# Optimization experiments

Hardware: AMD Instinct MI355X
Metric: run time of the kernel (lower is better)

The kernel has to match this reference:

```python
import jax, jax.numpy as jnp
import numpy as np

BS = 2048   # batch, iterated sequentially (memory carried step to step)
M = 256     # memory_size
E = 128     # expanded_memory_emb_size
HS = 512    # summarizer_hidden_size
HA = 512    # shared_AC_hidden_size
HP = 256    # processor_hidden_size


def make_pe(max_len, d):
    # standard sinusoidal positional encoding [max_len, d]
    pos = np.arange(max_len, dtype=np.float32)[:, None]
    div = np.exp(np.arange(0, d, 2, dtype=np.float32) * (-np.log(10000.0) / d))
    pe = np.zeros((max_len, d), dtype=np.float32)
    pe[:, 0::2] = np.sin(pos * div)
    pe[:, 1::2] = np.cos(pos * div)
    return jnp.asarray(pe)


def setup_inputs() -> dict:
    key = jax.random.key(0)
    ks = jax.random.split(key, 32)

    def n(k, sh, s=0.05):
        return jax.random.normal(k, sh, dtype=jnp.float32) * s

    return {
        "state": jax.random.normal(ks[0], (BS, 4), dtype=jnp.float32),
        "memory0": jax.random.uniform(ks[1], (M, E), dtype=jnp.float32),  # buffer init U(0,1)
        # embedder: Linear(4, E)
        "W_emb": n(ks[2], (4, E)), "b_emb": n(ks[3], (E,)),
        # reader Summarizer MLP: E -> HS -> 1
        "Wr1": n(ks[4], (E, HS)), "br1": n(ks[5], (HS,)),
        "Wr2": n(ks[6], (HS, 1)), "br2": n(ks[7], (1,)),
        # writer Summarizer MLP: E -> HS -> M
        "Ww1": n(ks[8], (E, HS)), "bw1": n(ks[9], (HS,)),
        "Ww2": n(ks[10], (HS, M)), "bw2": n(ks[11], (M,)),
        # shared AC trunk: 2E -> HA
        "Ws": n(ks[12], (2 * E, HA)), "bs_": n(ks[13], (HA,)),
        # actor: HA -> 5, critic: HA -> 1
        "Wa": n(ks[14], (HA, 5)), "ba": n(ks[15], (5,)),
        "Wc": n(ks[16], (HA, 1)), "bc": n(ks[17], (1,)),
        # processor: (5 + 1 + 2E) -> HP -> E
        "Wp1": n(ks[18], (5 + 1 + 2 * E, HP)), "bp1": n(ks[19], (HP,)),
        "Wp2": n(ks[20], (HP, E)), "bp2": n(ks[21], (E,)),
    }


def reference(state, memory0, W_emb, b_emb, Wr1, br1, Wr2, br2,
              Ww1, bw1, Ww2, bw2, Ws, bs_, Wa, ba, Wc, bc,
              Wp1, bp1, Wp2, bp2):
    pe_mem = make_pe(M, E)  # PE added to the M memory slots
    sg = jax.lax.stop_gradient

    def summarize(x, W1, b1, W2, b2):
        # Summarizer (MLP method): weight = softmax over token axis, z = weight^T x
        w = jax.nn.softmax(jax.nn.relu(x @ W1 + b1) @ W2 + b2, axis=0)  # [T, K]
        return w.T @ x  # [K, E]

    se = state @ W_emb + b_emb  # embed once: [BS, E]

    def step(mem, s):
        # reader over [current state ; PE(memory)] -> single summary token
        xr = jnp.concatenate([s[None, :], mem + pe_mem], axis=0)        # [M+1, E]
        mem_state = summarize(xr, Wr1, br1, Wr2, br2)[0]                # [E]
        cstate = jnp.concatenate([s, mem_state])                        # concat=True -> [2E]
        h = jax.nn.relu(cstate @ Ws + bs_)                              # [HA]
        probs = jax.nn.softmax(h @ Wa + ba)                             # [5]
        val = h @ Wc + bc                                               # [1]
        pin = jnp.concatenate([s, mem_state, probs, val])               # [2E+6]
        ms2 = jax.nn.relu(pin @ Wp1 + bp1) @ Wp2 + bp2                  # processed mem_state [E]
        # writer sees detached state / mem_state / memory (torch .detach())
        xw = jnp.concatenate([sg(s)[None, :], sg(ms2)[None, :], sg(mem) + pe_mem], axis=0)  # [M+2, E]
        nm = summarize(xw, Ww1, bw1, Ww2, bw2)                          # [M, E]
        nm = nm - nm.min(axis=-1, keepdims=True)
        nm = nm / nm.max(axis=-1, keepdims=True)
        return nm, (probs, val)

    _, (action_probs, state_values) = jax.lax.scan(step, memory0, se)
    return action_probs, state_values  # [BS, 5], [BS, 1]
```

## Files before the change

kernel.cpp:

```cpp
#include <hip/hip_runtime.h>
#include <math.h>

#define BSZ 2048
#define MM  256
#define EE  128
#define HSS 512
#define HPP 256
#define NOWN 64
#define NBLK 129
#define LEADER 128
#define TPB 512
#define ROWS 4

typedef float f4 __attribute__((ext_vector_type(4)));

#define OFF_PE   512
#define OFF_R0   (OFF_PE + MM*EE)
#define OFF_W0   (OFF_R0 + BSZ)
#define OFF_MP   (OFF_W0 + BSZ*MM)
#define OFF_SW   (OFF_MP + 2*MM*EE)
#define OFF_EV   (OFF_SW + 2*MM*MM)
#define OFF_ES   (OFF_EV + NOWN*EE)
#define OFF_MS2  (OFF_ES + NOWN)
#define OFF_CS   (OFF_MS2 + EE)
#define OFF_CBS  (OFF_CS + 4*HSS)
#define OFF_CP   (OFF_CBS + HSS)
#define OFF_CBP  (OFF_CP + 4*HPP)
#define OFF_BD   (OFF_CBP + HPP)
#define OFF_BP   (OFF_BD + NOWN*ROWS)

struct KParams {
  const float *state, *mem0, *Wemb, *bemb, *Wr1, *br1, *Wr2, *br2;
  const float *Ww1, *bw1, *Ww2, *bw2, *Ws, *bs, *Wa, *ba, *Wc, *bc;
  const float *Wp1, *bp1, *Wp2, *bp2;
  float *out;
  float *ws;
};

__device__ __forceinline__ float ldA(const float* p) {
  return __hip_atomic_load(p, __ATOMIC_RELAXED, __HIP_MEMORY_SCOPE_AGENT);
}
__device__ __forceinline__ void stA(float* p, float v) {
  __hip_atomic_store(p, v, __ATOMIC_RELAXED, __HIP_MEMORY_SCOPE_AGENT);
}
__device__ __forceinline__ unsigned ldAu(const unsigned* p) {
  return __hip_atomic_load(p, __ATOMIC_RELAXED, __HIP_MEMORY_SCOPE_AGENT);
}
__device__ __forceinline__ void stAu(unsigned* p, unsigned v) {
  __hip_atomic_store(p, v, __ATOMIC_RELAXED, __HIP_MEMORY_SCOPE_AGENT);
}

__device__ __forceinline__ void ldA4x8(const float* p, int strideF, f4* v) {
  const float *p1=p+strideF, *p2=p+2*strideF, *p3=p+3*strideF,
              *p4=p+4*strideF, *p5=p+5*strideF, *p6=p+6*strideF, *p7=p+7*strideF;
  asm volatile(
    "global_load_dwordx4 %0, %8, off sc0 sc1\n\t"
    "global_load_dwordx4 %1, %9, off sc0 sc1\n\t"
    "global_load_dwordx4 %2, %10, off sc0 sc1\n\t"
    "global_load_dwordx4 %3, %11, off sc0 sc1\n\t"
    "global_load_dwordx4 %4, %12, off sc0 sc1\n\t"
    "global_load_dwordx4 %5, %13, off sc0 sc1\n\t"
    "global_load_dwordx4 %6, %14, off sc0 sc1\n\t"
    "global_load_dwordx4 %7, %15, off sc0 sc1\n\t"
    "s_waitcnt vmcnt(0)"
    : "=&v"(v[0]), "=&v"(v[1]), "=&v"(v[2]), "=&v"(v[3]),
      "=&v"(v[4]), "=&v"(v[5]), "=&v"(v[6]), "=&v"(v[7])
    : "v"(p), "v"(p1), "v"(p2), "v"(p3), "v"(p4), "v"(p5), "v"(p6), "v"(p7)
    : "memory");
}
__device__ __forceinline__ void ldA4x4(const float* p, int strideF, f4* v) {
  const float *p1=p+strideF, *p2=p+2*strideF, *p3=p+3*strideF;
  asm volatile(
    "global_load_dwordx4 %0, %4, off sc0 sc1\n\t"
    "global_load_dwordx4 %1, %5, off sc0 sc1\n\t"
    "global_load_dwordx4 %2, %6, off sc0 sc1\n\t"
    "global_load_dwordx4 %3, %7, off sc0 sc1\n\t"
    "s_waitcnt vmcnt(0)"
    : "=&v"(v[0]), "=&v"(v[1]), "=&v"(v[2]), "=&v"(v[3])
    : "v"(p), "v"(p1), "v"(p2), "v"(p3)
    : "memory");
}
__device__ __forceinline__ f4 ldA4(const float* p) {
  f4 r;
  asm volatile("global_load_dwordx4 %0, %1, off sc0 sc1\n\ts_waitcnt vmcnt(0)"
    : "=&v"(r) : "v"(p) : "memory");
  return r;
}

__device__ __forceinline__ void drainSync() {
  asm volatile("s_waitcnt vmcnt(0)" ::: "memory");
  __syncthreads();
}

__device__ __forceinline__ float brs(float v, float* s8, int tid) {
  for (int o = 32; o > 0; o >>= 1) v += __shfl_down(v, o, 64);
  __syncthreads();
  if ((tid & 63) == 0) s8[tid >> 6] = v;
  __syncthreads();
  float r = s8[0]+s8[1]+s8[2]+s8[3]+s8[4]+s8[5]+s8[6]+s8[7];
  __syncthreads();
  return r;
}

template<int N>
__device__ __forceinline__ void brsN(float* v, float* sred, int tid) {
  #pragma unroll
  for (int k = 0; k < N; ++k)
    for (int o = 32; o > 0; o >>= 1) v[k] += __shfl_down(v[k], o, 64);
  __syncthreads();
  if ((tid & 63) == 0) {
    const int w = tid >> 6;
    #pragma unroll
    for (int k = 0; k < N; ++k) sred[k*8 + w] = v[k];
  }
  __syncthreads();
  #pragma unroll
  for (int k = 0; k < N; ++k) {
    float s = sred[k*8 + 0];
    #pragma unroll
    for (int w = 1; w < 8; ++w) s += sred[k*8 + w];
    v[k] = s;
  }
  __syncthreads();
}

__global__ __launch_bounds__(TPB)
void toyac_kernel(KParams p) {
  const int g = blockIdx.x;
  const int tid = threadIdx.x;
  float* ws = p.ws;
  unsigned* bar = (unsigned*)p.ws;
  const int og = (g >= NOWN && g < LEADER) ? (g - NOWN) : g;
  const int c0 = ROWS * ((g < NOWN) ? g : og);

  __shared__ float sX[ROWS][EE];
  __shared__ float sBuf[8192];
  __shared__ float sH4[ROWS][HSS];
  __shared__ float sHms[HSS];
  __shared__ float sEv[ROWS][MM];
  __shared__ float sRed[16];
  __shared__ float s8[8];
  __shared__ float sR48[48];
  __shared__ float sMS[EE];
  __shared__ float sMS2[EE];
  __shared__ float sSE[EE];
  __shared__ float sP1[HPP];
  __shared__ float sHv[HSS];
  __shared__ float sD[ROWS];
  __shared__ float sSm[32];

  const int hq = (tid & 127) * 4;
  const int eg4 = tid >> 7;

  if (g < NOWN) {
    const int e = tid & 127, r = tid >> 7, c = c0 + r;
    double dv = exp(-(double)(2*(e>>1)) * log(10000.0) / 128.0);
    double arg = (double)c * dv;
    float pev = ((e & 1) == 0) ? (float)sin(arg) : (float)cos(arg);
    ws[OFF_PE + (size_t)c*EE + e] = pev;
    float m0v = p.mem0[(size_t)c*EE + e] + pev;
    stA(ws + OFF_MP + (size_t)c*EE + e, m0v);
    sX[r][e] = m0v;
  } else if (g == LEADER) {
    for (int jj = tid; jj < HSS; jj += TPB) {
      float a0=0.f,a1=0.f,a2=0.f,a3=0.f,cb=0.f;
      for (int e = 0; e < EE; ++e) {
        float wv = p.Ws[(size_t)e*HSS + jj];
        a0 += p.Wemb[e]*wv; a1 += p.Wemb[EE+e]*wv;
        a2 += p.Wemb[2*EE+e]*wv; a3 += p.Wemb[3*EE+e]*wv;
        cb += p.bemb[e]*wv;
      }
      ws[OFF_CS + jj] = a0; ws[OFF_CS + HSS + jj] = a1;
      ws[OFF_CS + 2*HSS + jj] = a2; ws[OFF_CS + 3*HSS + jj] = a3;
      ws[OFF_CBS + jj] = cb;
    }
    if (tid < HPP) {
      int k = tid;
      float a0=0.f,a1=0.f,a2=0.f,a3=0.f,cb=0.f;
      for (int e = 0; e < EE; ++e) {
        float wv = p.Wp1[(size_t)e*HPP + k];
        a0 += p.Wemb[e]*wv; a1 += p.Wemb[EE+e]*wv;
        a2 += p.Wemb[2*EE+e]*wv; a3 += p.Wemb[3*EE+e]*wv;
        cb += p.bemb[e]*wv;
      }
      ws[OFF_CP + k] = a0; ws[OFF_CP + HPP + k] = a1;
      ws[OFF_CP + 2*HPP + k] = a2; ws[OFF_CP + 3*HPP + k] = a3;
      ws[OFF_CBP + k] = cb;
    }
  }

  for (int t = g; t < BSZ; t += NBLK) {
    __syncthreads();
    if (tid < EE) {
      const float* st = p.state + (size_t)t*4;
      sSE[tid] = st[0]*p.Wemb[tid] + st[1]*p.Wemb[EE+tid]
               + st[2]*p.Wemb[2*EE+tid] + st[3]*p.Wemb[3*EE+tid] + p.bemb[tid];
    }
    __syncthreads();
    {
      f4 a = {0.f,0.f,0.f,0.f};
      const float* base = p.Wr1 + (size_t)(eg4*32)*HSS + hq;
      for (int i = 0; i < 32; ++i)
        a += sSE[eg4*32 + i] * (*(const f4*)(base + (size_t)i*HSS));
      *(f4*)(sBuf + (size_t)eg4*HSS + hq) = a;
      __syncthreads();
      int h = tid;
      float hid = sBuf[h] + sBuf[HSS+h] + sBuf[2*HSS+h] + sBuf[3*HSS+h] + p.br1[h];
      float v = fmaxf(hid, 0.f) * p.Wr2[h];
      float sc = brs(v, s8, tid);
      if (tid == 0) stA(ws + OFF_R0 + t, sc + p.br2[0]);
      __syncthreads();
    }
    {
      f4 a = {0.f,0.f,0.f,0.f};
      const float* base = p.Ww1 + (size_t)(eg4*32)*HSS + hq;
      for (int i = 0; i < 32; ++i)
        a += sSE[eg4*32 + i] * (*(const f4*)(base + (size_t)i*HSS));
      *(f4*)(sBuf + (size_t)eg4*HSS + hq) = a;
      __syncthreads();
      int h = tid;
      sHv[h] = fmaxf(sBuf[h] + sBuf[HSS+h] + sBuf[2*HSS+h] + sBuf[3*HSS+h] + p.bw1[h], 0.f);
      __syncthreads();
      const int cq = (tid & 63) * 4, hg = tid >> 6;
      f4 q = {0.f,0.f,0.f,0.f};
      const float* b2 = p.Ww2 + (size_t)(hg*64)*MM + cq;
      for (int i = 0; i < 64; ++i)
        q += sHv[hg*64 + i] * (*(const f4*)(b2 + (size_t)i*MM));
      *(f4*)(sBuf + (size_t)hg*MM + cq) = q;
      __syncthreads();
      if (tid < MM) {
        float s = 0.f;
        #pragma unroll
        for (int k = 0; k < 8; ++k) s += sBuf[(size_t)k*MM + tid];
        stA(ws + OFF_W0 + (size_t)t*MM + tid, s + p.bw2[tid]);
      }
      __syncthreads();
    }
  }

  auto stageA = [&]() {
    {
      f4 a0={0.f,0.f,0.f,0.f},a1=a0,a2=a0,a3=a0;
      const float* base = p.Wr1 + (size_t)(eg4*32)*HSS + hq;
      for (int i = 0; i < 32; ++i) {
        f4 w = *(const f4*)(base + (size_t)i*HSS);
        int e = eg4*32 + i;
        a0 += sX[0][e]*w; a1 += sX[1][e]*w; a2 += sX[2][e]*w; a3 += sX[3][e]*w;
      }
      *(f4*)(sBuf + ((size_t)eg4*ROWS + 0)*HSS + hq) = a0;
      *(f4*)(sBuf + ((size_t)eg4*ROWS + 1)*HSS + hq) = a1;
      *(f4*)(sBuf + ((size_t)eg4*ROWS + 2)*HSS + hq) = a2;
      *(f4*)(sBuf + ((size_t)eg4*ROWS + 3)*HSS + hq) = a3;
    }
    __syncthreads();
    float es[ROWS];
    {
      int h = tid;
      float b = p.br1[h], wr = p.Wr2[h];
      float sc[ROWS];
      #pragma unroll
      for (int r = 0; r < ROWS; ++r) {
        float hid = sBuf[(0*ROWS+r)*HSS+h] + sBuf[(1*ROWS+r)*HSS+h]
                  + sBuf[(2*ROWS+r)*HSS+h] + sBuf[(3*ROWS+r)*HSS+h] + b;
        sc[r] = fmaxf(hid, 0.f) * wr;
      }
      brsN<ROWS>(sc, sR48, tid);
      #pragma unroll
      for (int r = 0; r < ROWS; ++r) es[r] = expf(sc[r] + p.br2[0]);
    }
    if (tid < EE) {
      float v = es[0]*sX[0][tid] + es[1]*sX[1][tid] + es[2]*sX[2][tid] + es[3]*sX[3][tid];
      stA(ws + OFF_EV + (size_t)g*EE + tid, v);
    }
    if (tid == 0) stA(ws + OFF_ES + g, es[0]+es[1]+es[2]+es[3]);
  };

  auto stageC = [&](float* swdst) {
    {
      f4 a0={0.f,0.f,0.f,0.f},a1=a0,a2=a0,a3=a0;
      const float* base = p.Ww1 + (size_t)(eg4*32)*HSS + hq;
      for (int i = 0; i < 32; ++i) {
        f4 w = *(const f4*)(base + (size_t)i*HSS);
        int e = eg4*32 + i;
        a0 += sX[0][e]*w; a1 += sX[1][e]*w; a2 += sX[2][e]*w; a3 += sX[3][e]*w;
      }
      *(f4*)(sBuf + ((size_t)eg4*ROWS + 0)*HSS + hq) = a0;
      *(f4*)(sBuf + ((size_t)eg4*ROWS + 1)*HSS + hq) = a1;
      *(f4*)(sBuf + ((size_t)eg4*ROWS + 2)*HSS + hq) = a2;
      *(f4*)(sBuf + ((size_t)eg4*ROWS + 3)*HSS + hq) = a3;
    }
    __syncthreads();
    {
      int h = tid;
      float b = p.bw1[h];
      #pragma unroll
      for (int r = 0; r < ROWS; ++r)
        sH4[r][h] = fmaxf(sBuf[(0*ROWS+r)*HSS+h] + sBuf[(1*ROWS+r)*HSS+h]
                        + sBuf[(2*ROWS+r)*HSS+h] + sBuf[(3*ROWS+r)*HSS+h] + b, 0.f);
    }
    __syncthreads();
    {
      const int cq = (tid & 63) * 4, hg = tid >> 6;
      f4 q0={0.f,0.f,0.f,0.f},q1=q0,q2=q0,q3=q0;
      const float* b2 = p.Ww2 + (size_t)(hg*64)*MM + cq;
      for (int i = 0; i < 64; ++i) {
        f4 w = *(const f4*)(b2 + (size_t)i*MM);
        int h = hg*64 + i;
        q0 += sH4[0][h]*w; q1 += sH4[1][h]*w; q2 += sH4[2][h]*w; q3 += sH4[3][h]*w;
      }
      *(f4*)(sBuf + ((size_t)hg*ROWS + 0)*MM + cq) = q0;
      *(f4*)(sBuf + ((size_t)hg*ROWS + 1)*MM + cq) = q1;
      *(f4*)(sBuf + ((size_t)hg*ROWS + 2)*MM + cq) = q2;
      *(f4*)(sBuf + ((size_t)hg*ROWS + 3)*MM + cq) = q3;
    }
    __syncthreads();
    {
      const int col = tid & 255, rp = tid >> 8;
      #pragma unroll
      for (int rr = 0; rr < 2; ++rr) {
        int r = rp*2 + rr;
        float s = 0.f;
        #pragma unroll
        for (int k = 0; k < 8; ++k) s += sBuf[((size_t)k*ROWS + r)*MM + col];
        stA(swdst + (size_t)(c0 + r)*MM + col, s + p.bw2[col]);
      }
    }
  };

  auto dBulkH = [&](int t) {
    float* swc = ws + OFF_SW + (size_t)(t&1)*MM*MM;
    float* mpc = ws + OFF_MP + (size_t)(t&1)*MM*EE;
    float ex[ROWS] = {0.f,0.f,0.f,0.f};
    if (tid < MM) {
      f4 s = ldA4(swc + (size_t)tid*MM + c0);
      #pragma unroll
      for (int r = 0; r < ROWS; ++r) { ex[r] = expf(s[r]); sEv[r][tid] = ex[r]; }
    }
    brsN<ROWS>(ex, sR48, tid);
    if (tid == 0) {
      stA(ws + OFF_BD + og*ROWS + 0, ex[0]);
      stA(ws + OFF_BD + og*ROWS + 1, ex[1]);
      stA(ws + OFF_BD + og*ROWS + 2, ex[2]);
      stA(ws + OFF_BD + og*ROWS + 3, ex[3]);
    }
    {
      const int e4 = (tid & 31) * 4, rg = tid >> 5;
      f4 a0={0.f,0.f,0.f,0.f},a1=a0,a2=a0,a3=a0;
      const float* base = mpc + (size_t)(rg*16)*EE + e4;
      f4 vv[8];
      ldA4x8(base, EE, vv);
      #pragma unroll
      for (int i = 0; i < 8; ++i) {
        int r0 = rg*16 + i;
        a0 += sEv[0][r0]*vv[i]; a1 += sEv[1][r0]*vv[i];
        a2 += sEv[2][r0]*vv[i]; a3 += sEv[3][r0]*vv[i];
      }
      ldA4x8(base + 8*EE, EE, vv);
      #pragma unroll
      for (int i = 0; i < 8; ++i) {
        int r0 = rg*16 + 8 + i;
        a0 += sEv[0][r0]*vv[i]; a1 += sEv[1][r0]*vv[i];
        a2 += sEv[2][r0]*vv[i]; a3 += sEv[3][r0]*vv[i];
      }
      *(f4*)(sBuf + ((size_t)0*16 + rg)*EE + e4) = a0;
      *(f4*)(sBuf + ((size_t)1*16 + rg)*EE + e4) = a1;
      *(f4*)(sBuf + ((size_t)2*16 + rg)*EE + e4) = a2;
      *(f4*)(sBuf + ((size_t)3*16 + rg)*EE + e4) = a3;
    }
    __syncthreads();
    {
      const int e = tid & 127, r = tid >> 7;
      float s = 0.f;
      #pragma unroll
      for (int q = 0; q < 16; ++q) s += sBuf[((size_t)r*16 + q)*EE + e];
      stA(ws + OFF_BP + ((size_t)og*ROWS + r)*EE + e, s);
    }
  };

  if (g == LEADER) {
    for (int t = 0; t < BSZ; ++t) {
      if (tid < NOWN) {
        while (ldAu(&bar[64+tid]) < (unsigned)(t+1)) __builtin_amdgcn_s_sleep(1);
      }
      __syncthreads();
      const float* st = p.state + (size_t)t*4;
      const float s0 = st[0], s1 = st[1], s2 = st[2], s3 = st[3];
      if (tid < EE)
        sSE[tid] = s0*p.Wemb[tid] + s1*p.Wemb[EE+tid]
                 + s2*p.Wemb[2*EE+tid] + s3*p.Wemb[3*EE+tid] + p.bemb[tid];
      float er0 = expf(ldA(ws + OFF_R0 + t));
      float v = (tid < NOWN) ? ldA(ws + OFF_ES + tid) : 0.f;
      float invd = 1.f / (er0 + brs(v, s8, tid));
      {
        const int e4 = (tid & 31) * 4, qg = tid >> 5;
        f4 vv[4];
        ldA4x4(ws + OFF_EV + (size_t)(qg*4)*EE + e4, EE, vv);
        f4 acc = vv[0]+vv[1]+vv[2]+vv[3];
        *(f4*)(sBuf + (size_t)qg*EE + e4) = acc;
      }
      __syncthreads();
      if (tid < EE) {
        float s = 0.f;
        #pragma unroll
        for (int q = 0; q < 16; ++q) s += sBuf[(size_t)q*EE + tid];
        sMS[tid] = (er0*sSE[tid] + s) * invd;
      }
      __syncthreads();
      {
        f4 a = {0.f,0.f,0.f,0.f};
        const float* base = p.Ws + (size_t)(EE + eg4*32)*HSS + hq;
        for (int i = 0; i < 32; ++i)
          a += sMS[eg4*32 + i] * (*(const f4*)(base + (size_t)i*HSS));
        *(f4*)(sBuf + (size_t)eg4*HSS + hq) = a;
      }
      __syncthreads();
      {
        int j = tid;
        const float* cs = ws + OFF_CS;
        float sh0 = s0*cs[j] + s1*cs[HSS+j] + s2*cs[2*HSS+j] + s3*cs[3*HSS+j] + ws[OFF_CBS + j];
        float hv = sBuf[j] + sBuf[HSS+j] + sBuf[2*HSS+j] + sBuf[3*HSS+j] + sh0 + p.bs[j];
        sHv[j] = fmaxf(hv, 0.f);
      }
      __syncthreads();
      {
        int j = tid;
        float hv = sHv[j];
        float pa[6];
        #pragma unroll
        for (int aa = 0; aa < 5; ++aa) pa[aa] = hv * p.Wa[(size_t)j*5 + aa];
        pa[5] = hv * p.Wc[j];
        brsN<6>(pa, sR48, tid);
        if (tid == 0) {
          float l0=pa[0]+p.ba[0], l1=pa[1]+p.ba[1], l2=pa[2]+p.ba[2];
          float l3=pa[3]+p.ba[3], l4=pa[4]+p.ba[4];
          float mx = fmaxf(fmaxf(fmaxf(l0,l1),fmaxf(l2,l3)), l4);
          float e0=expf(l0-mx),e1=expf(l1-mx),e2=expf(l2-mx),e3=expf(l3-mx),e4v=expf(l4-mx);
          float is = 1.f/(e0+e1+e2+e3+e4v);
          float p0=e0*is,p1=e1*is,p2=e2*is,p3=e3*is,p4=e4v*is;
          p.out[(size_t)t*5+0]=p0; p.out[(size_t)t*5+1]=p1; p.out[(size_t)t*5+2]=p2;
          p.out[(size_t)t*5+3]=p3; p.out[(size_t)t*5+4]=p4;
          float val = pa[5] + p.bc[0];
          p.out[(size_t)BSZ*5 + t] = val;
          sSm[1]=p0; sSm[2]=p1; sSm[3]=p2; sSm[4]=p3; sSm[5]=p4; sSm[6]=val;
        }
        __syncthreads();
      }
      {
        const int cq = (tid & 63) * 4, eg8 = tid >> 6;
        f4 a = {0.f,0.f,0.f,0.f};
        const float* base = p.Wp1 + (size_t)(EE + eg8*16)*HPP + cq;
        for (int i = 0; i < 16; ++i)
          a += sMS[eg8*16 + i] * (*(const f4*)(base + (size_t)i*HPP));
        *(f4*)(sBuf + (size_t)eg8*HPP + cq) = a;
      }
      __syncthreads();
      if (tid < HPP) {
        int k = tid;
        const float* cp = ws + OFF_CP;
        float acc = s0*cp[k] + s1*cp[HPP+k] + s2*cp[2*HPP+k] + s3*cp[3*HPP+k]
                  + ws[OFF_CBP + k] + p.bp1[k];
        #pragma unroll
        for (int q = 0; q < 8; ++q) acc += sBuf[(size_t)q*HPP + k];
        #pragma unroll
        for (int aa = 0; aa < 5; ++aa) acc += sSm[1+aa] * p.Wp1[(size_t)(2*EE+aa)*HPP + k];
        acc += sSm[6] * p.Wp1[(size_t)(2*EE+5)*HPP + k];
        sP1[k] = fmaxf(acc, 0.f);
      }
      __syncthreads();
      {
        const int cq = (tid & 31) * 4, kg = tid >> 5;
        f4 a = {0.f,0.f,0.f,0.f};
        const float* base = p.Wp2 + (size_t)(kg*16)*EE + cq;
        for (int i = 0; i < 16; ++i)
          a += sP1[kg*16 + i] * (*(const f4*)(base + (size_t)i*EE));
        *(f4*)(sBuf + (size_t)kg*EE + cq) = a;
      }
      __syncthreads();
      if (tid < EE) {
        float s = 0.f;
        #pragma unroll
        for (int q = 0; q < 16; ++q) s += sBuf[(size_t)q*EE + tid];
        stA(ws + OFF_MS2 + tid, s + p.bp2[tid]);
      }
      drainSync();
      if (tid == 0) stAu(&bar[320], (unsigned)(t+1));
    }
  } else if (g < NOWN) {
    const f4 wcol = *(const f4*)(p.Ww2 + (size_t)tid*MM + c0);
    drainSync();
    if (tid == 0) stAu(&bar[g], 1u);
    stageA();
    drainSync();
    if (tid == 0) stAu(&bar[64+g], 1u);

    for (int t = 0; t < BSZ-1; ++t) {
      if (tid < EE) {
        const float* st = p.state + (size_t)t*4;
        sSE[tid] = st[0]*p.Wemb[tid] + st[1]*p.Wemb[EE+tid]
                 + st[2]*p.Wemb[2*EE+tid] + st[3]*p.Wemb[3*EE+tid] + p.bemb[tid];
      }
      if (tid == 0) {
        f4 w0 = ldA4(ws + OFF_W0 + (size_t)t*MM + c0);
        #pragma unroll
        for (int r = 0; r < ROWS; ++r) sSm[8+r] = expf(w0[r]);
      }
      if (tid == 0) {
        while (ldAu(&bar[320]) < (unsigned)(t+1)) __builtin_amdgcn_s_sleep(1);
      }
      __syncthreads();
      if (tid < EE) sMS2[tid] = ldA(ws + OFF_MS2 + tid);
      __syncthreads();
      {
        f4 a = {0.f,0.f,0.f,0.f};
        const float* base = p.Ww1 + (size_t)(eg4*32)*HSS + hq;
        for (int i = 0; i < 32; ++i)
          a += sMS2[eg4*32 + i] * (*(const f4*)(base + (size_t)i*HSS));
        *(f4*)(sBuf + (size_t)eg4*HSS + hq) = a;
      }
      __syncthreads();
      sHms[tid] = fmaxf(sBuf[tid] + sBuf[HSS+tid] + sBuf[2*HSS+tid] + sBuf[3*HSS+tid]
                        + p.bw1[tid], 0.f);
      __syncthreads();
      float swv[ROWS];
      {
        float hm = sHms[tid];
        swv[0] = hm*wcol.x; swv[1] = hm*wcol.y; swv[2] = hm*wcol.z; swv[3] = hm*wcol.w;
        brsN<ROWS>(swv, sR48, tid);
      }
      if (tid == 0) {
        while (ldAu(&bar[192+g]) < (unsigned)(t+1)) __builtin_amdgcn_s_sleep(1);
      }
      __syncthreads();
      if (tid == 0) {
        f4 d = ldA4(ws + OFF_BD + g*ROWS);
        sD[0]=d.x; sD[1]=d.y; sD[2]=d.z; sD[3]=d.w;
      }
      __syncthreads();
      {
        const int e = tid & 127, r = tid >> 7;
        float bp = ldA(ws + OFF_BP + ((size_t)g*ROWS + r)*EE + e);
        float ew1 = expf(swv[r] + p.bw2[c0+r]);
        float ew0 = sSm[8+r];
        float inv = 1.f / (sD[r] + ew0 + ew1);
        float x = (bp + ew0*sSE[e] + ew1*sMS2[e]) * inv;
        float mn = x, mx = x;
        #pragma unroll
        for (int o = 1; o < 64; o <<= 1) {
          mn = fminf(mn, __shfl_xor(mn, o, 64));
          mx = fmaxf(mx, __shfl_xor(mx, o, 64));
        }
        if ((tid & 63) == 0) { sRed[(tid>>6)*2] = mn; sRed[(tid>>6)*2+1] = mx; }
        __syncthreads();
        mn = fminf(sRed[4*r], sRed[4*r+2]);
        mx = fmaxf(sRed[4*r+1], sRed[4*r+3]);
        float xr = (x - mn) / (mx - mn) + ws[OFF_PE + (size_t)(c0+r)*EE + e];
        float* mpn = ws + OFF_MP + (size_t)((t+1)&1)*MM*EE;
        stA(mpn + (size_t)(c0+r)*EE + e, xr);
        sX[r][e] = xr;
      }
      drainSync();
      if (tid == 0) stAu(&bar[g], (unsigned)(t+2));
      stageA();
      drainSync();
      if (tid == 0) stAu(&bar[64+g], (unsigned)(t+2));
    }
  } else {
    float* mpB[2] = { ws + OFF_MP, ws + OFF_MP + (size_t)MM*EE };
    for (int t = 0; t < BSZ-1; ++t) {
      if (tid == 0) {
        while (ldAu(&bar[og]) < (unsigned)(t+1)) __builtin_amdgcn_s_sleep(1);
      }
      __syncthreads();
      {
        const int e = tid & 127, r = tid >> 7;
        sX[r][e] = ldA(mpB[t&1] + (size_t)(c0+r)*EE + e);
      }
      __syncthreads();
      stageC(ws + OFF_SW + (size_t)(t&1)*MM*MM);
      drainSync();
      if (tid == 0) stAu(&bar[128+og], (unsigned)(t+1));
      if (tid < 64) {
        while (ldAu(&bar[128+tid]) < (unsigned)(t+1)) __builtin_amdgcn_s_sleep(1);
      } else if (tid < 128) {
        while (ldAu(&bar[tid-64]) < (unsigned)(t+1)) __builtin_amdgcn_s_sleep(1);
      }
      __syncthreads();
      dBulkH(t);
      drainSync();
      if (tid == 0) stAu(&bar[192+og], (unsigned)(t+1));
    }
  }
}

extern "C" void kernel_launch(void* const* d_in, const int* in_sizes, int n_in,
                              void* d_out, int out_size, void* d_ws, size_t ws_size,
                              hipStream_t stream) {
  hipMemsetAsync(d_ws, 0, 2048, stream);
  KParams kp;
  kp.state = (const float*)d_in[0];
  kp.mem0  = (const float*)d_in[1];
  kp.Wemb  = (const float*)d_in[2];
  kp.bemb  = (const float*)d_in[3];
  kp.Wr1   = (const float*)d_in[4];
  kp.br1   = (const float*)d_in[5];
  kp.Wr2   = (const float*)d_in[6];
  kp.br2   = (const float*)d_in[7];
  kp.Ww1   = (const float*)d_in[8];
  kp.bw1   = (const float*)d_in[9];
  kp.Ww2   = (const float*)d_in[10];
  kp.bw2   = (const float*)d_in[11];
  kp.Ws    = (const float*)d_in[12];
  kp.bs    = (const float*)d_in[13];
  kp.Wa    = (const float*)d_in[14];
  kp.ba    = (const float*)d_in[15];
  kp.Wc    = (const float*)d_in[16];
  kp.bc    = (const float*)d_in[17];
  kp.Wp1   = (const float*)d_in[18];
  kp.bp1   = (const float*)d_in[19];
  kp.Wp2   = (const float*)d_in[20];
  kp.bp2   = (const float*)d_in[21];
  kp.out   = (float*)d_out;
  kp.ws    = (float*)d_ws;
  toyac_kernel<<<dim3(NBLK), dim3(TPB), 0, stream>>>(kp);
}
```

Baseline: 54.94 ms.

## Replace counter barriers with padded data-carrying flags and hoist loads off critical path

Inter-block synchronisation now uses the data values themselves as ready flags: the per-block exp sums (ES) and denominators (BD) are written to cache-line-padded, double-buffered slots, polled until nonzero, then cleared. This removes separate counter barriers and an extra round trip per step. Barrier counters are spread onto separate 128-byte lines, positional encodings stay in shared memory, and the BP loads and the bw1 load are hoisted ahead of the critical waits. The owner spin on the leader flag no longer sleeps. The nonzero sentinel relies on the exponentials never being exactly zero, and spinning without sleep adds memory traffic.

Result: faster. 50.27 ms (-8.5%).

```diff
diff --git a/kernel.cpp b/kernel.cpp
--- a/kernel.cpp
+++ b/kernel.cpp
@@ -14,20 +14,23 @@
 
 typedef float f4 __attribute__((ext_vector_type(4)));
 
-#define OFF_PE   512
-#define OFF_R0   (OFF_PE + MM*EE)
-#define OFF_W0   (OFF_R0 + BSZ)
-#define OFF_MP   (OFF_W0 + BSZ*MM)
-#define OFF_SW   (OFF_MP + 2*MM*EE)
-#define OFF_EV   (OFF_SW + 2*MM*MM)
-#define OFF_ES   (OFF_EV + NOWN*EE)
-#define OFF_MS2  (OFF_ES + NOWN)
-#define OFF_CS   (OFF_MS2 + EE)
-#define OFF_CBS  (OFF_CS + 4*HSS)
-#define OFF_CP   (OFF_CBS + HSS)
-#define OFF_CBP  (OFF_CP + 4*HPP)
-#define OFF_BD   (OFF_CBP + HPP)
-#define OFF_BP   (OFF_BD + NOWN*ROWS)
+#define MSQ_IDX   0
+#define ROWQ(g)   ((1+(g))*32)
+#define SCQ(g)    ((65+(g))*32)
+#define OFF_ES    4160
+#define OFF_BD    8256
+#define OFF_PE    10304
+#define OFF_R0    (OFF_PE + MM*EE)
+#define OFF_W0    (OFF_R0 + BSZ)
+#define OFF_MP    (OFF_W0 + BSZ*MM)
+#define OFF_SW    (OFF_MP + 2*MM*EE)
+#define OFF_EV    (OFF_SW + 2*MM*MM)
+#define OFF_CS    (OFF_EV + NOWN*EE)
+#define OFF_CBS   (OFF_CS + 4*HSS)
+#define OFF_CP    (OFF_CBS + HSS)
+#define OFF_CBP   (OFF_CP + 4*HPP)
+#define OFF_MS2   (OFF_CBP + HPP)
+#define OFF_BP    (OFF_MS2 + EE)
 
 struct KParams {
   const float *state, *mem0, *Wemb, *bemb, *Wr1, *br1, *Wr2, *br2;
@@ -130,34 +133,37 @@
   const int tid = threadIdx.x;
   float* ws = p.ws;
   unsigned* bar = (unsigned*)p.ws;
+  const int isOwner = (g < NOWN);
   const int og = (g >= NOWN && g < LEADER) ? (g - NOWN) : g;
   const int c0 = ROWS * ((g < NOWN) ? g : og);
 
-  __shared__ float sX[ROWS][EE];
   __shared__ float sBuf[8192];
   __shared__ float sH4[ROWS][HSS];
-  __shared__ float sHms[HSS];
-  __shared__ float sEv[ROWS][MM];
-  __shared__ float sRed[16];
-  __shared__ float s8[8];
-  __shared__ float sR48[48];
+  __shared__ float sX[ROWS][EE];
+  __shared__ float sP[ROWS][EE];
+  __shared__ float sPE[ROWS][EE];
+  __shared__ float sHv[HSS];
   __shared__ float sMS[EE];
   __shared__ float sMS2[EE];
   __shared__ float sSE[EE];
   __shared__ float sP1[HPP];
-  __shared__ float sHv[HSS];
   __shared__ float sD[ROWS];
-  __shared__ float sSm[32];
+  __shared__ float sR48[48];
+  __shared__ float s8[8];
+  __shared__ float sRed[16];
+  __shared__ float sSm[40];
+
+  float (*sEv)[MM] = (float(*)[MM])sH4;
 
   const int hq = (tid & 127) * 4;
   const int eg4 = tid >> 7;
 
-  if (g < NOWN) {
+  if (isOwner) {
     const int e = tid & 127, r = tid >> 7, c = c0 + r;
     double dv = exp(-(double)(2*(e>>1)) * log(10000.0) / 128.0);
     double arg = (double)c * dv;
     float pev = ((e & 1) == 0) ? (float)sin(arg) : (float)cos(arg);
-    ws[OFF_PE + (size_t)c*EE + e] = pev;
+    sPE[r][e] = pev;
     float m0v = p.mem0[(size_t)c*EE + e] + pev;
     stA(ws + OFF_MP + (size_t)c*EE + e, m0v);
     sX[r][e] = m0v;
@@ -238,7 +244,7 @@
     }
   }
 
-  auto stageA = [&]() {
+  auto stageA = [&](float* esSumOut) {
     {
       f4 a0={0.f,0.f,0.f,0.f},a1=a0,a2=a0,a3=a0;
       const float* base = p.Wr1 + (size_t)(eg4*32)*HSS + hq;
@@ -253,11 +259,10 @@
       *(f4*)(sBuf + ((size_t)eg4*ROWS + 3)*HSS + hq) = a3;
     }
     __syncthreads();
-    float es[ROWS];
+    float sc[ROWS];
     {
       int h = tid;
       float b = p.br1[h], wr = p.Wr2[h];
-      float sc[ROWS];
       #pragma unroll
       for (int r = 0; r < ROWS; ++r) {
         float hid = sBuf[(0*ROWS+r)*HSS+h] + sBuf[(1*ROWS+r)*HSS+h]
@@ -265,54 +270,30 @@
         sc[r] = fmaxf(hid, 0.f) * wr;
       }
       brsN<ROWS>(sc, sR48, tid);
-      #pragma unroll
-      for (int r = 0; r < ROWS; ++r) es[r] = expf(sc[r] + p.br2[0]);
-    }
+    }
+    float es[ROWS];
+    #pragma unroll
+    for (int r = 0; r < ROWS; ++r) es[r] = expf(sc[r] + p.br2[0]);
     if (tid < EE) {
       float v = es[0]*sX[0][tid] + es[1]*sX[1][tid] + es[2]*sX[2][tid] + es[3]*sX[3][tid];
       stA(ws + OFF_EV + (size_t)g*EE + tid, v);
     }
-    if (tid == 0) stA(ws + OFF_ES + g, es[0]+es[1]+es[2]+es[3]);
+    *esSumOut = es[0]+es[1]+es[2]+es[3];
   };
 
-  auto stageC = [&](float* swdst) {
-    {
-      f4 a0={0.f,0.f,0.f,0.f},a1=a0,a2=a0,a3=a0;
-      const float* base = p.Ww1 + (size_t)(eg4*32)*HSS + hq;
-      for (int i = 0; i < 32; ++i) {
-        f4 w = *(const f4*)(base + (size_t)i*HSS);
-        int e = eg4*32 + i;
-        a0 += sX[0][e]*w; a1 += sX[1][e]*w; a2 += sX[2][e]*w; a3 += sX[3][e]*w;
-      }
-      *(f4*)(sBuf + ((size_t)eg4*ROWS + 0)*HSS + hq) = a0;
-      *(f4*)(sBuf + ((size_t)eg4*ROWS + 1)*HSS + hq) = a1;
-      *(f4*)(sBuf + ((size_t)eg4*ROWS + 2)*HSS + hq) = a2;
-      *(f4*)(sBuf + ((size_t)eg4*ROWS + 3)*HSS + hq) = a3;
-    }
-    __syncthreads();
-    {
-      int h = tid;
-      float b = p.bw1[h];
-      #pragma unroll
-      for (int r = 0; r < ROWS; ++r)
-        sH4[r][h] = fmaxf(sBuf[(0*ROWS+r)*HSS+h] + sBuf[(1*ROWS+r)*HSS+h]
-                        + sBuf[(2*ROWS+r)*HSS+h] + sBuf[(3*ROWS+r)*HSS+h] + b, 0.f);
-    }
-    __syncthreads();
-    {
-      const int cq = (tid & 63) * 4, hg = tid >> 6;
-      f4 q0={0.f,0.f,0.f,0.f},q1=q0,q2=q0,q3=q0;
-      const float* b2 = p.Ww2 + (size_t)(hg*64)*MM + cq;
-      for (int i = 0; i < 64; ++i) {
-        f4 w = *(const f4*)(b2 + (size_t)i*MM);
-        int h = hg*64 + i;
-        q0 += sH4[0][h]*w; q1 += sH4[1][h]*w; q2 += sH4[2][h]*w; q3 += sH4[3][h]*w;
-      }
-      *(f4*)(sBuf + ((size_t)hg*ROWS + 0)*MM + cq) = q0;
-      *(f4*)(sBuf + ((size_t)hg*ROWS + 1)*MM + cq) = q1;
-      *(f4*)(sBuf + ((size_t)hg*ROWS + 2)*MM + cq) = q2;
-      *(f4*)(sBuf + ((size_t)hg*ROWS + 3)*MM + cq) = q3;
-    }
+  auto ww2pass = [&](float* swdst) {
+    const int cq = (tid & 63) * 4, hg = tid >> 6;
+    f4 q0={0.f,0.f,0.f,0.f},q1=q0,q2=q0,q3=q0;
+    const float* b2 = p.Ww2 + (size_t)(hg*64)*MM + cq;
+    for (int i = 0; i < 64; ++i) {
+      f4 w = *(const f4*)(b2 + (size_t)i*MM);
+      int h = hg*64 + i;
+      q0 += sH4[0][h]*w; q1 += sH4[1][h]*w; q2 += sH4[2][h]*w; q3 += sH4[3][h]*w;
+    }
+    *(f4*)(sBuf + ((size_t)hg*ROWS + 0)*MM + cq) = q0;
+    *(f4*)(sBuf + ((size_t)hg*ROWS + 1)*MM + cq) = q1;
+    *(f4*)(sBuf + ((size_t)hg*ROWS + 2)*MM + cq) = q2;
+    *(f4*)(sBuf + ((size_t)hg*ROWS + 3)*MM + cq) = q3;
     __syncthreads();
     {
       const int col = tid & 255, rp = tid >> 8;
@@ -327,9 +308,36 @@
     }
   };
 
-  auto dBulkH = [&](int t) {
-    float* swc = ws + OFF_SW + (size_t)(t&1)*MM*MM;
-    float* mpc = ws + OFF_MP + (size_t)(t&1)*MM*EE;
+  auto stageC = [&](float* swdst) {
+    {
+      f4 a0={0.f,0.f,0.f,0.f},a1=a0,a2=a0,a3=a0;
+      const float* base = p.Ww1 + (size_t)(eg4*32)*HSS + hq;
+      for (int i = 0; i < 32; ++i) {
+        f4 w = *(const f4*)(base + (size_t)i*HSS);
+        int e = eg4*32 + i;
+        a0 += sX[0][e]*w; a1 += sX[1][e]*w; a2 += sX[2][e]*w; a3 += sX[3][e]*w;
+      }
+      *(f4*)(sBuf + ((size_t)eg4*ROWS + 0)*HSS + hq) = a0;
+      *(f4*)(sBuf + ((size_t)eg4*ROWS + 1)*HSS + hq) = a1;
+      *(f4*)(sBuf + ((size_t)eg4*ROWS + 2)*HSS + hq) = a2;
+      *(f4*)(sBuf + ((size_t)eg4*ROWS + 3)*HSS + hq) = a3;
+    }
+    __syncthreads();
+    {
+      int h = tid;
+      float b = p.bw1[h];
+      #pragma unroll
+      for (int r = 0; r < ROWS; ++r)
+        sH4[r][h] = fmaxf(sBuf[(0*ROWS+r)*HSS+h] + sBuf[(1*ROWS+r)*HSS+h]
+                        + sBuf[(2*ROWS+r)*HSS+h] + sBuf[(3*ROWS+r)*HSS+h] + b, 0.f);
+    }
+    __syncthreads();
+    ww2pass(swdst);
+  };
+
+  auto dBulkH = [&](int tt) {
+    float* swc = ws + OFF_SW + (size_t)(tt&1)*MM*MM;
+    float* mpc = ws + OFF_MP + (size_t)(tt&1)*MM*EE;
     float ex[ROWS] = {0.f,0.f,0.f,0.f};
     if (tid < MM) {
       f4 s = ldA4(swc + (size_t)tid*MM + c0);
@@ -337,12 +345,7 @@
       for (int r = 0; r < ROWS; ++r) { ex[r] = expf(s[r]); sEv[r][tid] = ex[r]; }
     }
     brsN<ROWS>(ex, sR48, tid);
-    if (tid == 0) {
-      stA(ws + OFF_BD + og*ROWS + 0, ex[0]);
-      stA(ws + OFF_BD + og*ROWS + 1, ex[1]);
-      stA(ws + OFF_BD + og*ROWS + 2, ex[2]);
-      stA(ws + OFF_BD + og*ROWS + 3, ex[3]);
-    }
+    if (tid == 0) { sD[0]=ex[0]; sD[1]=ex[1]; sD[2]=ex[2]; sD[3]=ex[3]; }
     {
       const int e4 = (tid & 31) * 4, rg = tid >> 5;
       f4 a0={0.f,0.f,0.f,0.f},a1=a0,a2=a0,a3=a0;
@@ -379,17 +382,13 @@
 
   if (g == LEADER) {
     for (int t = 0; t < BSZ; ++t) {
+      float er0 = expf(ldA(ws + OFF_R0 + t));
+      float v = 0.f;
       if (tid < NOWN) {
-        while (ldAu(&bar[64+tid]) < (unsigned)(t+1)) __builtin_amdgcn_s_sleep(1);
-      }
-      __syncthreads();
-      const float* st = p.state + (size_t)t*4;
-      const float s0 = st[0], s1 = st[1], s2 = st[2], s3 = st[3];
-      if (tid < EE)
-        sSE[tid] = s0*p.Wemb[tid] + s1*p.Wemb[EE+tid]
-                 + s2*p.Wemb[2*EE+tid] + s3*p.Wemb[3*EE+tid] + p.bemb[tid];
-      float er0 = expf(ldA(ws + OFF_R0 + t));
-      float v = (tid < NOWN) ? ldA(ws + OFF_ES + tid) : 0.f;
+        float* es = ws + OFF_ES + (size_t)((t&1)*NOWN + tid)*32;
+        do { v = ldA(es); } while (v == 0.f);
+        stA(es, 0.f);
+      }
       float invd = 1.f / (er0 + brs(v, s8, tid));
       {
         const int e4 = (tid & 31) * 4, qg = tid >> 5;
@@ -399,99 +398,105 @@
         *(f4*)(sBuf + (size_t)qg*EE + e4) = acc;
       }
       __syncthreads();
-      if (tid < EE) {
-        float s = 0.f;
-        #pragma unroll
-        for (int q = 0; q < 16; ++q) s += sBuf[(size_t)q*EE + tid];
-        sMS[tid] = (er0*sSE[tid] + s) * invd;
-      }
-      __syncthreads();
       {
-        f4 a = {0.f,0.f,0.f,0.f};
-        const float* base = p.Ws + (size_t)(EE + eg4*32)*HSS + hq;
-        for (int i = 0; i < 32; ++i)
-          a += sMS[eg4*32 + i] * (*(const f4*)(base + (size_t)i*HSS));
-        *(f4*)(sBuf + (size_t)eg4*HSS + hq) = a;
-      }
-      __syncthreads();
-      {
-        int j = tid;
-        const float* cs = ws + OFF_CS;
-        float sh0 = s0*cs[j] + s1*cs[HSS+j] + s2*cs[2*HSS+j] + s3*cs[3*HSS+j] + ws[OFF_CBS + j];
-        float hv = sBuf[j] + sBuf[HSS+j] + sBuf[2*HSS+j] + sBuf[3*HSS+j] + sh0 + p.bs[j];
-        sHv[j] = fmaxf(hv, 0.f);
-      }
-      __syncthreads();
-      {
-        int j = tid;
-        float hv = sHv[j];
-        float pa[6];
-        #pragma unroll
-        for (int aa = 0; aa < 5; ++aa) pa[aa] = hv * p.Wa[(size_t)j*5 + aa];
-        pa[5] = hv * p.Wc[j];
-        brsN<6>(pa, sR48, tid);
-        if (tid == 0) {
-          float l0=pa[0]+p.ba[0], l1=pa[1]+p.ba[1], l2=pa[2]+p.ba[2];
-          float l3=pa[3]+p.ba[3], l4=pa[4]+p.ba[4];
-          float mx = fmaxf(fmaxf(fmaxf(l0,l1),fmaxf(l2,l3)), l4);
-          float e0=expf(l0-mx),e1=expf(l1-mx),e2=expf(l2-mx),e3=expf(l3-mx),e4v=expf(l4-mx);
-          float is = 1.f/(e0+e1+e2+e3+e4v);
-          float p0=e0*is,p1=e1*is,p2=e2*is,p3=e3*is,p4=e4v*is;
-          p.out[(size_t)t*5+0]=p0; p.out[(size_t)t*5+1]=p1; p.out[(size_t)t*5+2]=p2;
-          p.out[(size_t)t*5+3]=p3; p.out[(size_t)t*5+4]=p4;
-          float val = pa[5] + p.bc[0];
-          p.out[(size_t)BSZ*5 + t] = val;
-          sSm[1]=p0; sSm[2]=p1; sSm[3]=p2; sSm[4]=p3; sSm[5]=p4; sSm[6]=val;
+        const float* st = p.state + (size_t)t*4;
+        const float s0 = st[0], s1 = st[1], s2 = st[2], s3 = st[3];
+        if (tid < EE) {
+          float se = s0*p.Wemb[tid] + s1*p.Wemb[EE+tid]
+                   + s2*p.Wemb[2*EE+tid] + s3*p.Wemb[3*EE+tid] + p.bemb[tid];
+          float s = 0.f;
+          #pragma unroll
+          for (int q = 0; q < 16; ++q) s += sBuf[(size_t)q*EE + tid];
+          sMS[tid] = (er0*se + s) * invd;
         }
         __syncthreads();
-      }
-      {
-        const int cq = (tid & 63) * 4, eg8 = tid >> 6;
-        f4 a = {0.f,0.f,0.f,0.f};
-        const float* base = p.Wp1 + (size_t)(EE + eg8*16)*HPP + cq;
-        for (int i = 0; i < 16; ++i)
-          a += sMS[eg8*16 + i] * (*(const f4*)(base + (size_t)i*HPP));
-        *(f4*)(sBuf + (size_t)eg8*HPP + cq) = a;
-      }
-      __syncthreads();
-      if (tid < HPP) {
-        int k = tid;
-        const float* cp = ws + OFF_CP;
-        float acc = s0*cp[k] + s1*cp[HPP+k] + s2*cp[2*HPP+k] + s3*cp[3*HPP+k]
-                  + ws[OFF_CBP + k] + p.bp1[k];
-        #pragma unroll
-        for (int q = 0; q < 8; ++q) acc += sBuf[(size_t)q*HPP + k];
-        #pragma unroll
-        for (int aa = 0; aa < 5; ++aa) acc += sSm[1+aa] * p.Wp1[(size_t)(2*EE+aa)*HPP + k];
-        acc += sSm[6] * p.Wp1[(size_t)(2*EE+5)*HPP + k];
-        sP1[k] = fmaxf(acc, 0.f);
-      }
-      __syncthreads();
-      {
-        const int cq = (tid & 31) * 4, kg = tid >> 5;
-        f4 a = {0.f,0.f,0.f,0.f};
-        const float* base = p.Wp2 + (size_t)(kg*16)*EE + cq;
-        for (int i = 0; i < 16; ++i)
-          a += sP1[kg*16 + i] * (*(const f4*)(base + (size_t)i*EE));
-        *(f4*)(sBuf + (size_t)kg*EE + cq) = a;
-      }
-      __syncthreads();
-      if (tid < EE) {
-        float s = 0.f;
-        #pragma unroll
-        for (int q = 0; q < 16; ++q) s += sBuf[(size_t)q*EE + tid];
-        stA(ws + OFF_MS2 + tid, s + p.bp2[tid]);
+        {
+          f4 a = {0.f,0.f,0.f,0.f};
+          const float* base = p.Ws + (size_t)(EE + eg4*32)*HSS + hq;
+          for (int i = 0; i < 32; ++i)
+            a += sMS[eg4*32 + i] * (*(const f4*)(base + (size_t)i*HSS));
+          *(f4*)(sBuf + (size_t)eg4*HSS + hq) = a;
+        }
+        __syncthreads();
+        float hv;
+        {
+          const float* cs = ws + OFF_CS;
+          float sh0 = s0*cs[tid] + s1*cs[HSS+tid] + s2*cs[2*HSS+tid] + s3*cs[3*HSS+tid]
+                    + ws[OFF_CBS + tid];
+          hv = fmaxf(sBuf[tid] + sBuf[HSS+tid] + sBuf[2*HSS+tid] + sBuf[3*HSS+tid]
+                     + sh0 + p.bs[tid], 0.f);
+        }
+        __syncthreads();
+        {
+          float pa[6];
+          #pragma unroll
+          for (int aa = 0; aa < 5; ++aa) pa[aa] = hv * p.Wa[(size_t)tid*5 + aa];
+          pa[5] = hv * p.Wc[tid];
+          brsN<6>(pa, sR48, tid);
+          if (tid == 0) {
+            float l0=pa[0]+p.ba[0], l1=pa[1]+p.ba[1], l2=pa[2]+p.ba[2];
+            float l3=pa[3]+p.ba[3], l4=pa[4]+p.ba[4];
+            float mx = fmaxf(fmaxf(fmaxf(l0,l1),fmaxf(l2,l3)), l4);
+            float e0=expf(l0-mx),e1=expf(l1-mx),e2=expf(l2-mx),e3=expf(l3-mx),e4v=expf(l4-mx);
+            float is = 1.f/(e0+e1+e2+e3+e4v);
+            float p0=e0*is,p1=e1*is,p2=e2*is,p3=e3*is,p4=e4v*is;
+            p.out[(size_t)t*5+0]=p0; p.out[(size_t)t*5+1]=p1; p.out[(size_t)t*5+2]=p2;
+            p.out[(size_t)t*5+3]=p3; p.out[(size_t)t*5+4]=p4;
+            float val = pa[5] + p.bc[0];
+            p.out[(size_t)BSZ*5 + t] = val;
+            sSm[1]=p0; sSm[2]=p1; sSm[3]=p2; sSm[4]=p3; sSm[5]=p4; sSm[6]=val;
+          }
+          __syncthreads();
+        }
+        {
+          const int cq = (tid & 63) * 4, eg8 = tid >> 6;
+          f4 a = {0.f,0.f,0.f,0.f};
+          const float* base = p.Wp1 + (size_t)(EE + eg8*16)*HPP + cq;
+          for (int i = 0; i < 16; ++i)
+            a += sMS[eg8*16 + i] * (*(const f4*)(base + (size_t)i*HPP));
+          *(f4*)(sBuf + (size_t)eg8*HPP + cq) = a;
+        }
+        __syncthreads();
+        if (tid < HPP) {
+          const float* cp = ws + OFF_CP;
+          float acc = s0*cp[tid] + s1*cp[HPP+tid] + s2*cp[2*HPP+tid] + s3*cp[3*HPP+tid]
+                    + ws[OFF_CBP + tid] + p.bp1[tid];
+          #pragma unroll
+          for (int q = 0; q < 8; ++q) acc += sBuf[(size_t)q*HPP + tid];
+          #pragma unroll
+          for (int aa = 0; aa < 5; ++aa) acc += sSm[1+aa] * p.Wp1[(size_t)(2*EE+aa)*HPP + tid];
+          acc += sSm[6] * p.Wp1[(size_t)(2*EE+5)*HPP + tid];
+          sP1[tid] = fmaxf(acc, 0.f);
+        }
+        __syncthreads();
+        {
+          const int cq = (tid & 31) * 4, kg = tid >> 5;
+          f4 a = {0.f,0.f,0.f,0.f};
+          const float* base = p.Wp2 + (size_t)(kg*16)*EE + cq;
+          for (int i = 0; i < 16; ++i)
+            a += sP1[kg*16 + i] * (*(const f4*)(base + (size_t)i*EE));
+          *(f4*)(sBuf + (size_t)kg*EE + cq) = a;
+        }
+        __syncthreads();
+        if (tid < EE) {
+          float s = 0.f;
+          #pragma unroll
+          for (int q = 0; q < 16; ++q) s += sBuf[(size_t)q*EE + tid];
+          stA(ws + OFF_MS2 + tid, s + p.bp2[tid]);
+        }
       }
       drainSync();
-      if (tid == 0) stAu(&bar[320], (unsigned)(t+1));
-    }
-  } else if (g < NOWN) {
+      if (tid == 0) stAu(&bar[MSQ_IDX], (unsigned)(t+1));
+    }
+  } else if (isOwner) {
     const f4 wcol = *(const f4*)(p.Ww2 + (size_t)tid*MM + c0);
+    const float rBw1v = p.bw1[tid];
     drainSync();
-    if (tid == 0) stAu(&bar[g], 1u);
-    stageA();
+    if (tid == 0) stAu(&bar[ROWQ(g)], 1u);
+    float esSum;
+    stageA(&esSum);
     drainSync();
-    if (tid == 0) stAu(&bar[64+g], 1u);
+    if (tid == 0) stA(ws + OFF_ES + (size_t)g*32, esSum);
 
     for (int t = 0; t < BSZ-1; ++t) {
       if (tid < EE) {
@@ -501,15 +506,24 @@
       }
       if (tid == 0) {
         f4 w0 = ldA4(ws + OFF_W0 + (size_t)t*MM + c0);
-        #pragma unroll
-        for (int r = 0; r < ROWS; ++r) sSm[8+r] = expf(w0[r]);
-      }
+        sSm[8]=expf(w0.x); sSm[9]=expf(w0.y); sSm[10]=expf(w0.z); sSm[11]=expf(w0.w);
+      }
+      if (tid == 0) { while (ldAu(&bar[MSQ_IDX]) < (unsigned)(t+1)) {} }
+      __syncthreads();
+      if (tid < EE) sMS2[tid] = ldA(ws + OFF_MS2 + tid);
       if (tid == 0) {
-        while (ldAu(&bar[320]) < (unsigned)(t+1)) __builtin_amdgcn_s_sleep(1);
-      }
-      __syncthreads();
-      if (tid < EE) sMS2[tid] = ldA(ws + OFF_MS2 + tid);
-      __syncthreads();
+        float* bd = ws + OFF_BD + (size_t)g*32;
+        float x,y,z,w;
+        do { x=ldA(bd); y=ldA(bd+1); z=ldA(bd+2); w=ldA(bd+3); }
+        while (x==0.f || y==0.f || z==0.f || w==0.f);
+        sD[0]=x; sD[1]=y; sD[2]=z; sD[3]=w;
+        stA(bd,0.f); stA(bd+1,0.f); stA(bd+2,0.f); stA(bd+3,0.f);
+      }
+      __syncthreads();
+      {
+        const int e = tid & 127, r = tid >> 7;
+        sP[r][e] = ldA(ws + OFF_BP + ((size_t)g*ROWS + r)*EE + e);
+      }
       {
         f4 a = {0.f,0.f,0.f,0.f};
         const float* base = p.Ww1 + (size_t)(eg4*32)*HSS + hq;
@@ -518,31 +532,17 @@
         *(f4*)(sBuf + (size_t)eg4*HSS + hq) = a;
       }
       __syncthreads();
-      sHms[tid] = fmaxf(sBuf[tid] + sBuf[HSS+tid] + sBuf[2*HSS+tid] + sBuf[3*HSS+tid]
-                        + p.bw1[tid], 0.f);
-      __syncthreads();
-      float swv[ROWS];
-      {
-        float hm = sHms[tid];
-        swv[0] = hm*wcol.x; swv[1] = hm*wcol.y; swv[2] = hm*wcol.z; swv[3] = hm*wcol.w;
-        brsN<ROWS>(swv, sR48, tid);
-      }
-      if (tid == 0) {
-        while (ldAu(&bar[192+g]) < (unsigned)(t+1)) __builtin_amdgcn_s_sleep(1);
-      }
-      __syncthreads();
-      if (tid == 0) {
-        f4 d = ldA4(ws + OFF_BD + g*ROWS);
-        sD[0]=d.x; sD[1]=d.y; sD[2]=d.z; sD[3]=d.w;
-      }
-      __syncthreads();
+      float hm = fmaxf(sBuf[tid] + sBuf[HSS+tid] + sBuf[2*HSS+tid] + sBuf[3*HSS+tid]
+                       + rBw1v, 0.f);
+      __syncthreads();
+      float swv[ROWS] = { hm*wcol.x, hm*wcol.y, hm*wcol.z, hm*wcol.w };
+      brsN<ROWS>(swv, sR48, tid);
       {
         const int e = tid & 127, r = tid >> 7;
-        float bp = ldA(ws + OFF_BP + ((size_t)g*ROWS + r)*EE + e);
         float ew1 = expf(swv[r] + p.bw2[c0+r]);
         float ew0 = sSm[8+r];
         float inv = 1.f / (sD[r] + ew0 + ew1);
-        float x = (bp + ew0*sSE[e] + ew1*sMS2[e]) * inv;
+        float x = (sP[r][e] + ew0*sSE[e] + ew1*sMS2[e]) * inv;
         float mn = x, mx = x;
         #pragma unroll
         for (int o = 1; o < 64; o <<= 1) {
@@ -553,41 +553,44 @@
         __syncthreads();
         mn = fminf(sRed[4*r], sRed[4*r+2]);
         mx = fmaxf(sRed[4*r+1], sRed[4*r+3]);
-        float xr = (x - mn) / (mx - mn) + ws[OFF_PE + (size_t)(c0+r)*EE + e];
-        float* mpn = ws + OFF_MP + (size_t)((t+1)&1)*MM*EE;
-        stA(mpn + (size_t)(c0+r)*EE + e, xr);
+        float k = 1.f / (mx - mn);
+        float xr = (x - mn) * k + sPE[r][e];
+        stA(ws + OFF_MP + (size_t)((t+1)&1)*MM*EE + (size_t)(c0+r)*EE + e, xr);
         sX[r][e] = xr;
       }
       drainSync();
-      if (tid == 0) stAu(&bar[g], (unsigned)(t+2));
-      stageA();
+      if (tid == 0) stAu(&bar[ROWQ(g)], (unsigned)(t+2));
+      stageA(&esSum);
       drainSync();
-      if (tid == 0) stAu(&bar[64+g], (unsigned)(t+2));
+      if (tid == 0) stA(ws + OFF_ES + (size_t)(((t+1)&1)*NOWN + g)*32, esSum);
     }
   } else {
-    float* mpB[2] = { ws + OFF_MP, ws + OFF_MP + (size_t)MM*EE };
     for (int t = 0; t < BSZ-1; ++t) {
       if (tid == 0) {
-        while (ldAu(&bar[og]) < (unsigned)(t+1)) __builtin_amdgcn_s_sleep(1);
+        while (ldAu(&bar[ROWQ(og)]) < (unsigned)(t+1)) __builtin_amdgcn_s_sleep(2);
       }
       __syncthreads();
       {
         const int e = tid & 127, r = tid >> 7;
-        sX[r][e] = ldA(mpB[t&1] + (size_t)(c0+r)*EE + e);
+        sX[r][e] = ldA(ws + OFF_MP + (size_t)(t&1)*MM*EE + (size_t)(c0+r)*EE + e);
       }
       __syncthreads();
       stageC(ws + OFF_SW + (size_t)(t&1)*MM*MM);
       drainSync();
-      if (tid == 0) stAu(&bar[128+og], (unsigned)(t+1));
+      if (tid == 0) stAu(&bar[SCQ(og)], (unsigned)(t+1));
       if (tid < 64) {
-        while (ldAu(&bar[128+tid]) < (unsigned)(t+1)) __builtin_amdgcn_s_sleep(1);
+        while (ldAu(&bar[SCQ(tid)]) < (unsigned)(t+1)) __builtin_amdgcn_s_sleep(2);
       } else if (tid < 128) {
-        while (ldAu(&bar[tid-64]) < (unsigned)(t+1)) __builtin_amdgcn_s_sleep(1);
+        while (ldAu(&bar[ROWQ(tid-64)]) < (unsigned)(t+1)) __builtin_amdgcn_s_sleep(2);
       }
       __syncthreads();
       dBulkH(t);
       drainSync();
-      if (tid == 0) stAu(&bar[192+og], (unsigned)(t+1));
+      if (tid == 0) {
+        float* bd = ws + OFF_BD + (size_t)og*32;
+        stA(bd,   sD[0]); stA(bd+1, sD[1]);
+        stA(bd+2, sD[2]); stA(bd+3, sD[3]);
+      }
     }
   }
 }
@@ -595,7 +598,7 @@
 extern "C" void kernel_launch(void* const* d_in, const int* in_sizes, int n_in,
                               void* d_out, int out_size, void* d_ws, size_t ws_size,
                               hipStream_t stream) {
-  hipMemsetAsync(d_ws, 0, 2048, stream);
+  hipMemsetAsync(d_ws, 0, OFF_PE * 4, stream);
   KParams kp;
   kp.state = (const float*)d_in[0];
   kp.mem0  = (const float*)d_in[1];
```
